# Optimization experiments

Measured on AMD Instinct MI355X. Metric: run time of the kernel, lower is better.

Reference implementation:

```python
import jax, jax.numpy as jnp
import numpy as np

ALPHA = 0.2   # LeakyReLU slope
NEG = -9e15   # masked-attention fill, as in standard dense GAT


def _gat_multihead(h, edge_attr, adj, n2n, Wg, Weg, a_s, a_d, a_e, concat):
    # h: [N, I], edge_attr: [E, I], adj: [N, N], n2n: [N*N, I]
    # Wg, Weg: [H, I, O]; a_s, a_d, a_e: [H, O]
    H, I, O = Wg.shape
    N = h.shape[0]
    Wh = jnp.einsum('ni,hio->hno', h, Wg)                    # [H, N, O]
    es = jnp.einsum('hno,ho->hn', Wh, a_s)                   # [H, N] source logits
    ed = jnp.einsum('hno,ho->hn', Wh, a_d)                   # [H, N] dest logits
    ve = jnp.einsum('hio,ho->hi', Weg, a_e)                  # [H, I] fold edge proj into vector
    ee = (n2n @ ve.T).T.reshape(H, N, N)                     # [H, N, N] edge logits (row=src)
    e = jax.nn.leaky_relu(es[:, :, None] + ed[:, None, :] + ee, ALPHA)
    e = jnp.where(adj[None] > 0, e, NEG)
    attn = jax.nn.softmax(e, axis=-1)
    hout = jnp.einsum('hnm,hmo->nho', attn, Wh).reshape(N, H * O)
    eout = jnp.einsum('ei,hio->eho', edge_attr, Weg).reshape(-1, H * O)
    if concat:
        hout, eout = jax.nn.elu(hout), jax.nn.elu(eout)
    return hout, eout


def _edge_pool(x, edge_index, edge_attr, Wp, bp):
    # Deterministic static-shape variant of EdgePooling: merge node pairs (2k, 2k+1)
    # with a learned sigmoid score over the concatenated endpoint features.
    N, F = x.shape
    x2 = x.reshape(N // 2, 2, F)
    score = jax.nn.sigmoid(jnp.concatenate([x2[:, 0], x2[:, 1]], axis=1) @ Wp + bp)  # [N/2,1]
    new_x = (x2[:, 0] + x2[:, 1]) * score
    return new_x, edge_index // 2, edge_attr


def _global_attn(x, W, b):
    # GlobalAttention with gate_nn = Linear -> Sigmoid, softmax over the single graph
    gate = jax.nn.sigmoid(x @ W + b)          # [N, 1]
    alpha = jax.nn.softmax(gate, axis=0)
    return (alpha * x).sum(axis=0, keepdims=True)  # [1, F]


def _adj_n2n(N, edge_index, edge_attr):
    # Faithful vectorized version of _get_adj_node2node (scatter replaces python loop)
    src, dst = edge_index[0], edge_index[1]
    adj = jnp.zeros((N, N), edge_attr.dtype).at[src, dst].add(1.0)
    n2n = jnp.zeros((N * N, edge_attr.shape[1]), edge_attr.dtype).at[src * N + dst].set(edge_attr)
    return adj, n2n


def setup_inputs() -> dict:
    key = jax.random.key(0)
    ks = jax.random.split(key, 24)
    N, E, HID, NH = 512, 4096, 64, 16
    O = 2 * HID                                  # per-head GAT output = 128
    CAT = NH * O                                 # 2048
    s = 0.1
    features = jax.random.normal(ks[0], (N, HID), jnp.float32)
    edge_index = jax.random.randint(ks[1], (2, E), 0, N, jnp.int64)
    edge_attr = jax.random.normal(ks[2], (E, HID), jnp.float32)
    adjacency, n2n = _adj_n2n(N, edge_index, edge_attr)
    inp = dict(features=features, edge_index=edge_index, edge_attr=edge_attr,
               adjacency=adjacency, n2n=n2n)
    # SingleNodeAttentionLayer params
    inp['W_sn'] = jax.random.normal(ks[3], (HID, HID), jnp.float32) * s
    inp['a_sn'] = jax.random.normal(ks[4], (HID,), jnp.float32) * s
    # 16-head GAT layer (stacked over heads)
    inp['Wg'] = jax.random.normal(ks[5], (NH, HID, O), jnp.float32) * s
    inp['Weg'] = jax.random.normal(ks[6], (NH, HID, O), jnp.float32) * s
    inp['a_src'] = jax.random.normal(ks[7], (NH, O), jnp.float32) * s
    inp['a_dst'] = jax.random.normal(ks[8], (NH, O), jnp.float32) * s
    inp['a_edge'] = jax.random.normal(ks[9], (NH, O), jnp.float32) * s
    # edge_pool1 (in = NH*O = 2048)
    inp['Wp1'] = jax.random.normal(ks[10], (2 * CAT, 1), jnp.float32) * s
    inp['bp1'] = jnp.zeros((1,), jnp.float32)
    # out_att single head: 2048 -> 128
    inp['Wo'] = jax.random.normal(ks[11], (CAT, O), jnp.float32) * s
    inp['Weo'] = jax.random.normal(ks[12], (CAT, O), jnp.float32) * s
    inp['ao_src'] = jax.random.normal(ks[13], (O,), jnp.float32) * s
    inp['ao_dst'] = jax.random.normal(ks[14], (O,), jnp.float32) * s
    inp['ao_edge'] = jax.random.normal(ks[15], (O,), jnp.float32) * s
    # edge_pool2 (in = O = 128)
    inp['Wp2'] = jax.random.normal(ks[16], (2 * O, 1), jnp.float32) * s
    inp['bp2'] = jnp.zeros((1,), jnp.float32)
    # global-attention gates
    inp['g1W'] = jax.random.normal(ks[17], (HID, 1), jnp.float32) * s
    inp['g1b'] = jnp.zeros((1,), jnp.float32)
    inp['g2W'] = jax.random.normal(ks[18], (CAT, 1), jnp.float32) * s
    inp['g2b'] = jnp.zeros((1,), jnp.float32)
    inp['g3W'] = jax.random.normal(ks[19], (O, 1), jnp.float32) * s
    inp['g3b'] = jnp.zeros((1,), jnp.float32)
    return inp


def reference(features, edge_index, edge_attr, adjacency, n2n,
              W_sn, a_sn, Wg, Weg, a_src, a_dst, a_edge, Wp1, bp1,
              Wo, Weo, ao_src, ao_dst, ao_edge, Wp2, bp2,
              g1W, g1b, g2W, g2b, g3W, g3b):
    # SingleNodeAttentionLayer: per-node gated projection
    Wh0 = features @ W_sn
    coef = jax.nn.sigmoid(jax.nn.leaky_relu(Wh0 @ a_sn, ALPHA))
    h = jax.nn.elu(coef[:, None] * Wh0)                       # [N, HID]
    hs = [_global_attn(h, g1W, g1b)]
    # 16-head GAT (dropout inactive: training=False)
    h, ea = _gat_multihead(h, edge_attr, adjacency, n2n, Wg, Weg, a_src, a_dst, a_edge, True)
    h, ei, ea = _edge_pool(h, edge_index, ea, Wp1, bp1)
    hs.append(_global_attn(h, g2W, g2b))
    # rebuild dense adjacency + node2node features (scatter)
    adj2, n2n2 = _adj_n2n(h.shape[0], ei, ea)
    h, ea = _gat_multihead(h, ea, adj2, n2n2, Wo[None], Weo[None],
                           ao_src[None], ao_dst[None], ao_edge[None], False)
    h, ei, ea = _edge_pool(h, ei, ea, Wp2, bp2)
    hs.append(_global_attn(h, g3W, g3b))
    return jnp.concatenate(hs, axis=1)                        # [1, 64+2048+128]
```

## Files before the change

### kernel.cpp

```cpp
#include <hip/hip_runtime.h>
#include <hip/hip_bf16.h>

__device__ __forceinline__ float sigm(float x) { return 1.f / (1.f + expf(-x)); }
__device__ __forceinline__ float lrelu(float x) { return x > 0.f ? x : 0.2f * x; }
__device__ __forceinline__ float eluf(float x) { return x > 0.f ? x : expf(x) - 1.f; }

#define NEGF (-9e15f)
#define MAXD 40

__device__ __forceinline__ float wave_sum(float v) {
    #pragma unroll
    for (int off = 32; off >= 1; off >>= 1) v += __shfl_xor(v, off);
    return v;
}
__device__ __forceinline__ float wave_max(float v) {
    #pragma unroll
    for (int off = 32; off >= 1; off >>= 1) v = fmaxf(v, __shfl_xor(v, off));
    return v;
}
__device__ __forceinline__ float half_sum(float v) {
    #pragma unroll
    for (int off = 16; off >= 1; off >>= 1) v += __shfl_xor(v, off);
    return v;
}
__device__ __forceinline__ float half_max(float v) {
    #pragma unroll
    for (int off = 16; off >= 1; off >>= 1) v = fmaxf(v, __shfl_xor(v, off));
    return v;
}

__global__ void k_setup(const float* __restrict__ Wg, const float* __restrict__ Weg,
                        const float* __restrict__ asrc, const float* __restrict__ adst,
                        const float* __restrict__ aedge, const float* __restrict__ Weo,
                        const float* __restrict__ aoe,
                        const float* __restrict__ feat, const float* __restrict__ Wsn,
                        const float* __restrict__ asn, const float* __restrict__ g1W,
                        const float* __restrict__ g1b,
                        float* __restrict__ vs1, float* __restrict__ vd1, float* __restrict__ ve1,
                        float* __restrict__ ve2, int* __restrict__ winner,
                        float* __restrict__ h, float* __restrict__ gate1) {
    int b = blockIdx.x, t = threadIdx.x, w = t >> 6, l = t & 63;
    __shared__ float fr[4][64];
    if (b < 16) {
        int hd = b;
        float s0 = asrc[hd * 128 + l],  s1 = asrc[hd * 128 + 64 + l];
        float d0 = adst[hd * 128 + l],  d1 = adst[hd * 128 + 64 + l];
        float e0 = aedge[hd * 128 + l], e1 = aedge[hd * 128 + 64 + l];
        for (int i = w; i < 64; i += 4) {
            const float* Wr = Wg  + ((size_t)hd * 64 + i) * 128;
            const float* Er = Weg + ((size_t)hd * 64 + i) * 128;
            float w1 = Wr[l], w2 = Wr[64 + l];
            float q1 = Er[l], q2 = Er[64 + l];
            float pS = wave_sum(w1 * s0 + w2 * s1);
            float pD = wave_sum(w1 * d0 + w2 * d1);
            float pE = wave_sum(q1 * e0 + q2 * e1);
            if (l == 0) { vs1[hd * 64 + i] = pS; vd1[hd * 64 + i] = pD; ve1[hd * 64 + i] = pE; }
        }
    } else if (b < 32) {
        int base = (b - 16) * 128;
        float a0 = aoe[l], a1 = aoe[64 + l];
        for (int k = 0; k < 32; k++) {
            int c = base + w * 32 + k;
            const float* Wr = Weo + (size_t)c * 128;
            float p = wave_sum(Wr[l] * a0 + Wr[64 + l] * a1);
            if (l == 0) ve2[c] = p;
        }
    } else if (b < 48) {
        int base = (b - 32) * 4096;
        #pragma unroll
        for (int k = 0; k < 16; k++) winner[base + k * 256 + t] = -1;
    } else {
        int n = (b - 48) * 4 + w;
        fr[w][l] = feat[n * 64 + l];
        __syncthreads();
        float acc = 0.f;
        #pragma unroll 8
        for (int i = 0; i < 64; i++) acc += fr[w][i] * Wsn[i * 64 + l];
        float p = wave_sum(acc * asn[l]);
        float coef = sigm(lrelu(p));
        float hv = eluf(coef * acc);
        h[n * 64 + l] = hv;
        float g = wave_sum(hv * g1W[l]);
        if (l == 0) gate1[n] = sigm(g + g1b[0]);
    }
}

__global__ void k_mid(const float* __restrict__ h, const float* __restrict__ gate,
                      const float* __restrict__ vs1, const float* __restrict__ vd1,
                      const int* __restrict__ ei,
                      float* __restrict__ part1, float* __restrict__ es1, float* __restrict__ ed1,
                      int* __restrict__ winner) {
    int b = blockIdx.x, t = threadIdx.x;
    if (b < 8) {
        int nb = b, w = t >> 6, l = t & 63;
        __shared__ float mx[8], sm[8], al[512], pt[8][64];
        float g = gate[t];
        float m = wave_max(g);
        if (l == 0) mx[w] = m;
        __syncthreads();
        m = mx[0];
        #pragma unroll
        for (int i = 1; i < 8; i++) m = fmaxf(m, mx[i]);
        float p = expf(g - m);
        float Z = wave_sum(p);
        if (l == 0) sm[w] = Z;
        __syncthreads();
        Z = 0.f;
        #pragma unroll
        for (int i = 0; i < 8; i++) Z += sm[i];
        al[t] = p / Z;
        __syncthreads();
        int r0 = nb * 64 + w * 8;
        float acc = 0.f;
        #pragma unroll
        for (int r = 0; r < 8; r++) acc += al[r0 + r] * h[(r0 + r) * 64 + l];
        pt[w][l] = acc;
        __syncthreads();
        if (t < 64) {
            float o = 0.f;
            #pragma unroll
            for (int q = 0; q < 8; q++) o += pt[q][t];
            part1[nb * 64 + t] = o;
        }
    } else if (b < 24) {
        __shared__ float vsT[64][17], vdT[64][17];
        for (int idx = t; idx < 1024; idx += 512) {
            int i = idx & 63, hd = idx >> 6;
            vsT[i][hd] = vs1[hd * 64 + i];
            vdT[i][hd] = vd1[hd * 64 + i];
        }
        __syncthreads();
        int idx = (b - 8) * 512 + t;
        int n = idx >> 4, hd = idx & 15;
        const float* hr = h + n * 64;
        float aS = 0.f, aD = 0.f;
        #pragma unroll 8
        for (int i = 0; i < 64; i++) {
            float hv = hr[i];
            aS += hv * vsT[i][hd];
            aD += hv * vdT[i][hd];
        }
        es1[hd * 512 + n] = aS;
        ed1[hd * 512 + n] = aD;
    } else {
        int e = (b - 24) * 512 + t;
        int s = ei[e] >> 1, d = ei[4096 + e] >> 1;
        atomicMax(&winner[s * 256 + d], e);
    }
}

__global__ void k_attn_ze(const float* __restrict__ adj, const float* __restrict__ n2n,
                          const float* __restrict__ h, const float* __restrict__ ve1,
                          const float* __restrict__ es1, const float* __restrict__ ed1,
                          const float* __restrict__ eattr, const float* __restrict__ Weg,
                          const float* __restrict__ ve2,
                          float* __restrict__ z, float* __restrict__ d2) {
    int b = blockIdx.x, t = threadIdx.x, w = t >> 6, l = t & 63;
    if (b >= 512) {
        int e0 = (b - 512) * 8;
        int hd = t >> 5, q = t & 31;
        __shared__ float ea[8][64];
        __shared__ float sd2[8][8];
        ea[t >> 6][t & 63] = eattr[(size_t)(e0 + (t >> 6)) * 64 + (t & 63)];
        __syncthreads();
        float4 acc[8];
        #pragma unroll
        for (int r = 0; r < 8; r++) acc[r] = make_float4(0.f, 0.f, 0.f, 0.f);
        const float4* W4 = (const float4*)Weg + (size_t)hd * 2048 + q;
        #pragma unroll 4
        for (int i = 0; i < 64; i++) {
            float4 wv = W4[i * 32];
            #pragma unroll
            for (int r = 0; r < 8; r++) {
                float a = ea[r][i];
                acc[r].x += a * wv.x; acc[r].y += a * wv.y;
                acc[r].z += a * wv.z; acc[r].w += a * wv.w;
            }
        }
        float4 v2 = ((const float4*)ve2)[hd * 32 + q];
        #pragma unroll
        for (int r = 0; r < 8; r++) {
            float p = eluf(acc[r].x) * v2.x + eluf(acc[r].y) * v2.y
                    + eluf(acc[r].z) * v2.z + eluf(acc[r].w) * v2.w;
            p = wave_sum(p);
            if (l == 0) sd2[r][w] = p;
        }
        __syncthreads();
        if (t < 8) {
            float s8 = 0.f;
            #pragma unroll
            for (int k = 0; k < 8; k++) s8 += sd2[t][k];
            d2[e0 + t] = s8;
        }
        return;
    }
    int s = b;
    __shared__ float vlT[64][17];
    __shared__ float hrow[MAXD][65], nrow[MAXD][65];
    __shared__ float eh[16][48], ah[16][48];
    __shared__ float esr[16];
    __shared__ int dlist[MAXD];
    __shared__ int wbase[8];
    __shared__ int nnz_s;
    __shared__ float part[8][64];

    for (int idx = t; idx < 1024; idx += 512) vlT[idx & 63][idx >> 6] = ve1[(idx >> 6) * 64 + (idx & 63)];
    if (t < 16) esr[t] = es1[t * 512 + s];
    float a = adj[s * 512 + t];
    unsigned long long mask = __ballot(a > 0.f);
    if (l == 0) wbase[w] = __popcll(mask);
    __syncthreads();
    if (t == 0) {
        int run = 0;
        #pragma unroll
        for (int i = 0; i < 8; i++) { int c = wbase[i]; wbase[i] = run; run += c; }
        nnz_s = run;
    }
    __syncthreads();
    if (a > 0.f) {
        int slot = wbase[w] + __popcll(mask & ((1ULL << l) - 1ULL));
        if (slot < MAXD) dlist[slot] = t;
    }
    __syncthreads();
    int nnz = min(nnz_s, MAXD);

    if (nnz == 0) {
        int i = t & 63, q = t >> 6;
        float acc = 0.f;
        for (int d = q * 64; d < q * 64 + 64; d++) acc += h[d * 64 + i];
        part[q][i] = acc;
        __syncthreads();
        if (t < 64) {
            float sum = 0.f;
            #pragma unroll
            for (int q2 = 0; q2 < 8; q2++) sum += part[q2][t];
            float v = sum * (1.f / 512.f);
            for (int hd = 0; hd < 16; hd++) z[(size_t)s * 1024 + hd * 64 + t] = v;
        }
        return;
    }

    for (int base = 0; base < nnz; base += 8) {
        int j = base + (t >> 6);
        if (j < nnz) {
            int d = dlist[j];
            hrow[j][l] = h[d * 64 + l];
            nrow[j][l] = n2n[((size_t)s * 512 + d) * 64 + l];
        }
    }
    __syncthreads();
    for (int jb = 0; jb < nnz; jb += 32) {
        int j = jb + (t >> 4), hd = t & 15;
        if (j < nnz) {
            float ee = 0.f;
            #pragma unroll 8
            for (int i = 0; i < 64; i++) ee += nrow[j][i] * vlT[i][hd];
            eh[hd][j] = lrelu(esr[hd] + ed1[hd * 512 + dlist[j]] + ee);
        }
    }
    __syncthreads();
    {
        int hd = t >> 5, lane32 = t & 31;
        float v0 = (lane32 < nnz) ? eh[hd][lane32] : -1e30f;
        float v1 = (lane32 + 32 < nnz) ? eh[hd][lane32 + 32] : -1e30f;
        float m = half_max(fmaxf(v0, v1));
        float p0 = (lane32 < nnz) ? expf(v0 - m) : 0.f;
        float p1 = (lane32 + 32 < nnz) ? expf(v1 - m) : 0.f;
        float Z = half_sum(p0 + p1);
        float inv = 1.f / Z;
        if (lane32 < nnz) ah[hd][lane32] = p0 * inv;
        if (lane32 + 32 < nnz) ah[hd][lane32 + 32] = p1 * inv;
    }
    __syncthreads();
    int hd = t >> 5, i0 = t & 31;
    float a0 = 0.f, a1 = 0.f;
    for (int j = 0; j < nnz; j++) {
        float aj = ah[hd][j];
        a0 += aj * hrow[j][i0];
        a1 += aj * hrow[j][i0 + 32];
    }
    z[(size_t)s * 1024 + hd * 64 + i0]      = a0;
    z[(size_t)s * 1024 + hd * 64 + i0 + 32] = a1;
}

__global__ void k_houtg(const float* __restrict__ z, const float* __restrict__ Wg,
                        float* __restrict__ hout) {
    int sb = blockIdx.x, hd = blockIdx.y, c = threadIdx.x;
    __shared__ float zt[8][64];
    int s0 = sb * 8;
    for (int idx = c; idx < 512; idx += 128) {
        int r = idx >> 6, i = idx & 63;
        zt[r][i] = z[(size_t)(s0 + r) * 1024 + hd * 64 + i];
    }
    __syncthreads();
    float acc[8] = {0, 0, 0, 0, 0, 0, 0, 0};
    const float* W = Wg + (size_t)hd * 8192 + c;
    #pragma unroll 8
    for (int i = 0; i < 64; i++) {
        float wv = W[(size_t)i * 128];
        #pragma unroll
        for (int r = 0; r < 8; r++) acc[r] += zt[r][i] * wv;
    }
    #pragma unroll
    for (int r = 0; r < 8; r++)
        hout[(size_t)(s0 + r) * 2048 + hd * 128 + c] = eluf(acc[r]);
}

__global__ void k_pool1g2(const float* __restrict__ x, const float* __restrict__ Wp,
                          const float* __restrict__ bp, const float* __restrict__ g2W,
                          const float* __restrict__ g2b,
                          float* __restrict__ xo, float* __restrict__ gate2) {
    int k = blockIdx.x, t = threadIdx.x, w = t >> 6, l = t & 63;
    __shared__ float sd[4], sg[4];
    float p = 0.f;
    for (int f = t; f < 2048; f += 256)
        p += x[(size_t)(2 * k) * 2048 + f] * Wp[f] + x[(size_t)(2 * k + 1) * 2048 + f] * Wp[2048 + f];
    p = wave_sum(p);
    if (l == 0) sd[w] = p;
    __syncthreads();
    float sc = sigm(sd[0] + sd[1] + sd[2] + sd[3] + bp[0]);
    float pg = 0.f;
    for (int f = t; f < 2048; f += 256) {
        float v = x[(size_t)(2 * k) * 2048 + f] + x[(size_t)(2 * k + 1) * 2048 + f];
        xo[(size_t)k * 2048 + f] = v * sc;
        pg += v * g2W[f];
    }
    pg = wave_sum(pg);
    if (l == 0) sg[w] = pg;
    __syncthreads();
    if (t == 0) gate2[k] = sigm(sc * (sg[0] + sg[1] + sg[2] + sg[3]) + g2b[0]);
}

__global__ void k_big2(const float* __restrict__ x, const float* __restrict__ Wo,
                       const float* __restrict__ aos, const float* __restrict__ aod,
                       const float* __restrict__ gate2,
                       float* __restrict__ Wh2, float* __restrict__ es2, float* __restrict__ ed2,
                       float* __restrict__ part2) {
    int b = blockIdx.x, t = threadIdx.x;
    if (b < 128) {
        int n0 = b * 2;
        int ks = t >> 7, c = t & 127;
        __shared__ float xr[2][2048];
        __shared__ float part[8][2][128];
        __shared__ float rs[4], rd[4];
        for (int idx = t; idx < 4096; idx += 1024) xr[idx >> 11][idx & 2047] = x[(size_t)n0 * 2048 + idx];
        __syncthreads();
        float a0 = 0.f, a1 = 0.f;
        const float* W  = Wo + (size_t)(ks * 256) * 128 + c;
        const float* x0 = xr[0] + ks * 256;
        const float* x1 = xr[1] + ks * 256;
        #pragma unroll 8
        for (int i = 0; i < 256; i++) { float w = W[(size_t)i * 128]; a0 += x0[i] * w; a1 += x1[i] * w; }
        part[ks][0][c] = a0;
        part[ks][1][c] = a1;
        __syncthreads();
        if (t < 256) {
            int r = t >> 7, cc = t & 127;
            float a = 0.f;
            #pragma unroll
            for (int k = 0; k < 8; k++) a += part[k][r][cc];
            Wh2[(n0 + r) * 128 + cc] = a;
            float ps = wave_sum(a * aos[cc]);
            float pd = wave_sum(a * aod[cc]);
            if ((t & 63) == 0) { rs[t >> 6] = ps; rd[t >> 6] = pd; }
        }
        __syncthreads();
        if (t == 0) { es2[n0] = rs[0] + rs[1]; ed2[n0] = rd[0] + rd[1]; }
        if (t == 1) { es2[n0 + 1] = rs[2] + rs[3]; ed2[n0 + 1] = rd[2] + rd[3]; }
    } else {
        int wb = b - 128;
        int grp = t >> 8, tt = t & 255;
        int tile = wb * 4 + grp;
        int cb = tile >> 3, nb = tile & 7;
        __shared__ float mx[4][4], sm[4][4], al[4][256];
        int w4 = tt >> 6, l = tt & 63;
        float g = gate2[tt];
        float m = wave_max(g);
        if (l == 0) mx[grp][w4] = m;
        __syncthreads();
        m = fmaxf(fmaxf(mx[grp][0], mx[grp][1]), fmaxf(mx[grp][2], mx[grp][3]));
        float p = expf(g - m);
        float Z = wave_sum(p);
        if (l == 0) sm[grp][w4] = Z;
        __syncthreads();
        Z = sm[grp][0] + sm[grp][1] + sm[grp][2] + sm[grp][3];
        al[grp][tt] = p / Z;
        __syncthreads();
        int c = cb * 256 + tt;
        int n0 = nb * 32;
        float acc = 0.f;
        #pragma unroll 8
        for (int n = n0; n < n0 + 32; n++) acc += al[grp][n] * x[(size_t)n * 2048 + c];
        part2[nb * 2048 + c] = acc;
    }
}

__global__ void k_fin(const int* __restrict__ winner, const float* __restrict__ d2,
                      const float* __restrict__ es2, const float* __restrict__ ed2,
                      const float* __restrict__ Wh2, const float* __restrict__ part1,
                      const float* __restrict__ part2,
                      float* __restrict__ hout2, float* __restrict__ out) {
    int b = blockIdx.x, t = threadIdx.x;
    if (b < 256) {
        int s = b, w = t >> 6, l = t & 63;
        __shared__ float mx[4], sm[4], at[256], part[2][128];
        int win = winner[s * 256 + t];
        float e;
        if (win >= 0) e = lrelu(es2[s] + ed2[t] + d2[win]);
        else e = NEGF;
        float m = wave_max(e);
        if (l == 0) mx[w] = m;
        __syncthreads();
        m = fmaxf(fmaxf(mx[0], mx[1]), fmaxf(mx[2], mx[3]));
        float p = expf(e - m);
        float Z = wave_sum(p);
        if (l == 0) sm[w] = Z;
        __syncthreads();
        Z = sm[0] + sm[1] + sm[2] + sm[3];
        at[t] = p / Z;
        __syncthreads();
        int c = t & 127, hf = t >> 7;
        float acc = 0.f;
        for (int d = hf * 128; d < hf * 128 + 128; d++)
            acc += at[d] * Wh2[d * 128 + c];
        part[hf][c] = acc;
        __syncthreads();
        if (t < 128) hout2[s * 128 + t] = part[0][t] + part[1][t];
    } else if (b == 256) {
        if (t < 64) {
            float o = 0.f;
            #pragma unroll
            for (int nb = 0; nb < 8; nb++) o += part1[nb * 64 + t];
            out[t] = o;
        }
    } else {
        int c = (b - 257) * 256 + t;
        float o = 0.f;
        #pragma unroll
        for (int nb = 0; nb < 8; nb++) o += part2[nb * 2048 + c];
        out[64 + c] = o;
    }
}

__global__ void k_tail(const float* __restrict__ hout2, const float* __restrict__ Wp,
                       const float* __restrict__ bp, const float* __restrict__ g3W,
                       const float* __restrict__ g3b, float* __restrict__ out) {
    int t = threadIdx.x, w = t >> 6, l = t & 63;
    __shared__ float x2s[128][129];
    __shared__ float gt[128];
    __shared__ float mx[2], sm[2], al[128], part[4][128];
    float bpv = bp[0], g3bv = g3b[0];
    for (int rr = 0; rr < 16; rr++) {
        int k = w * 16 + rr;
        float a0  = hout2[(size_t)(2 * k) * 128 + l];
        float a0b = hout2[(size_t)(2 * k) * 128 + 64 + l];
        float a1  = hout2[(size_t)(2 * k + 1) * 128 + l];
        float a1b = hout2[(size_t)(2 * k + 1) * 128 + 64 + l];
        float p = a0 * Wp[l] + a0b * Wp[64 + l] + a1 * Wp[128 + l] + a1b * Wp[192 + l];
        p = wave_sum(p);
        float sc = sigm(p + bpv);
        float v  = (a0 + a1) * sc;
        float vb = (a0b + a1b) * sc;
        x2s[k][l] = v;
        x2s[k][64 + l] = vb;
        float g = wave_sum(v * g3W[l] + vb * g3W[64 + l]);
        if (l == 0) gt[k] = sigm(g + g3bv);
    }
    __syncthreads();
    if (t < 128) {
        float g = gt[t];
        float m = wave_max(g);
        if (l == 0) mx[w] = m;
    }
    __syncthreads();
    if (t < 128) {
        float g = gt[t];
        float m = fmaxf(mx[0], mx[1]);
        float p = expf(g - m);
        float Z = wave_sum(p);
        if (l == 0) sm[w] = Z;
        al[t] = p;
    }
    __syncthreads();
    float invZ = 1.f / (sm[0] + sm[1]);
    int q = t >> 7, c = t & 127;
    float acc = 0.f;
    for (int n = q * 32; n < q * 32 + 32; n++) acc += al[n] * x2s[n][c];
    part[q][c] = acc * invZ;
    __syncthreads();
    if (t < 128) out[2112 + t] = part[0][t] + part[1][t] + part[2][t] + part[3][t];
}

extern "C" void kernel_launch(void* const* d_in, const int* in_sizes, int n_in,
                              void* d_out, int out_size, void* d_ws, size_t ws_size,
                              hipStream_t stream) {
    const float* feat  = (const float*)d_in[0];
    const int*   eidx  = (const int*)d_in[1];
    const float* eattr = (const float*)d_in[2];
    const float* adj   = (const float*)d_in[3];
    const float* n2n   = (const float*)d_in[4];
    const float* Wsn   = (const float*)d_in[5];
    const float* asn   = (const float*)d_in[6];
    const float* Wg    = (const float*)d_in[7];
    const float* Weg   = (const float*)d_in[8];
    const float* asrc  = (const float*)d_in[9];
    const float* adst  = (const float*)d_in[10];
    const float* aedge = (const float*)d_in[11];
    const float* Wp1   = (const float*)d_in[12];
    const float* bp1   = (const float*)d_in[13];
    const float* Wo    = (const float*)d_in[14];
    const float* Weo   = (const float*)d_in[15];
    const float* aos   = (const float*)d_in[16];
    const float* aod   = (const float*)d_in[17];
    const float* aoe   = (const float*)d_in[18];
    const float* Wp2   = (const float*)d_in[19];
    const float* bp2   = (const float*)d_in[20];
    const float* g1W   = (const float*)d_in[21];
    const float* g1b   = (const float*)d_in[22];
    const float* g2W   = (const float*)d_in[23];
    const float* g2b   = (const float*)d_in[24];
    const float* g3W   = (const float*)d_in[25];
    const float* g3b   = (const float*)d_in[26];
    float* out = (float*)d_out;

    char* ws = (char*)d_ws;
    float* h      = (float*)(ws + 0x0000000);
    float* z      = (float*)(ws + 0x0020000);
    float* ve1    = (float*)(ws + 0x0430000);
    float* ve2    = (float*)(ws + 0x0431000);
    float* gate1  = (float*)(ws + 0x0433000);
    float* gate2  = (float*)(ws + 0x0434000);
    float* vs1    = (float*)(ws + 0x0436000);
    float* vd1    = (float*)(ws + 0x0438000);
    float* es1    = (float*)(ws + 0x0440000);
    float* ed1    = (float*)(ws + 0x0448000);
    float* hout1  = (float*)(ws + 0x1440000);
    float* d2     = (float*)(ws + 0x1840000);
    float* x1p    = (float*)(ws + 0x1850000);
    int*   winner = (int*)  (ws + 0x1A50000);
    float* Wh2    = (float*)(ws + 0x1A90000);
    float* es2    = (float*)(ws + 0x1AB0000);
    float* ed2    = (float*)(ws + 0x1AB1000);
    float* hout2  = (float*)(ws + 0x1AB2000);
    float* part2  = (float*)(ws + 0x1AE2000);
    float* part1  = (float*)(ws + 0x1AF2000);

    k_setup  <<<176, 256, 0, stream>>>(Wg, Weg, asrc, adst, aedge, Weo, aoe,
                                       feat, Wsn, asn, g1W, g1b,
                                       vs1, vd1, ve1, ve2, winner, h, gate1);
    k_mid    <<<32, 512, 0, stream>>>(h, gate1, vs1, vd1, eidx, part1, es1, ed1, winner);
    k_attn_ze<<<1024, 512, 0, stream>>>(adj, n2n, h, ve1, es1, ed1, eattr, Weg, ve2, z, d2);
    k_houtg  <<<dim3(64, 16), 128, 0, stream>>>(z, Wg, hout1);
    k_pool1g2<<<256, 256, 0, stream>>>(hout1, Wp1, bp1, g2W, g2b, x1p, gate2);
    k_big2   <<<144, 1024, 0, stream>>>(x1p, Wo, aos, aod, gate2, Wh2, es2, ed2, part2);
    k_fin    <<<265, 256, 0, stream>>>(winner, d2, es2, ed2, Wh2, part1, part2, hout2, out);
    k_tail   <<<1, 512, 0, stream>>>(hout2, Wp2, bp2, g3W, g3b, out);
}
```

Measured before the change: 130.9 us.

## Restage edge projection per head, fuse pool1 into big2, rebalance later kernels

The edge-projection branch of k_attn_ze now runs one block per (head, 256-edge chunk). Each block keeps that head's Weg slice in shared memory and writes per-head partial d2 values. k_houtg gains an extra row of blocks that reduces those partials across heads. k_pool1g2 is folded into k_big2p, so pooled rows come straight from shared memory instead of a separate launch. The global-attention partial sums move into k_fin and the final out reduction into extra k_tail blocks, which removes one launch at the cost of an extra workspace buffer and more shared memory per block.

```diff
diff --git a/kernel.cpp b/kernel.cpp
--- a/kernel.cpp
+++ b/kernel.cpp
@@ -154,55 +154,46 @@
                           const float* __restrict__ es1, const float* __restrict__ ed1,
                           const float* __restrict__ eattr, const float* __restrict__ Weg,
                           const float* __restrict__ ve2,
-                          float* __restrict__ z, float* __restrict__ d2) {
+                          float* __restrict__ z, float* __restrict__ d2p) {
     int b = blockIdx.x, t = threadIdx.x, w = t >> 6, l = t & 63;
+    __shared__ __align__(16) char smem[34816];
     if (b >= 512) {
-        int e0 = (b - 512) * 8;
-        int hd = t >> 5, q = t & 31;
-        __shared__ float ea[8][64];
-        __shared__ float sd2[8][8];
-        ea[t >> 6][t & 63] = eattr[(size_t)(e0 + (t >> 6)) * 64 + (t & 63)];
-        __syncthreads();
-        float4 acc[8];
-        #pragma unroll
-        for (int r = 0; r < 8; r++) acc[r] = make_float4(0.f, 0.f, 0.f, 0.f);
-        const float4* W4 = (const float4*)Weg + (size_t)hd * 2048 + q;
-        #pragma unroll 4
-        for (int i = 0; i < 64; i++) {
-            float4 wv = W4[i * 32];
-            #pragma unroll
-            for (int r = 0; r < 8; r++) {
-                float a = ea[r][i];
-                acc[r].x += a * wv.x; acc[r].y += a * wv.y;
-                acc[r].z += a * wv.z; acc[r].w += a * wv.w;
+        float (*Wl)[128] = reinterpret_cast<float(*)[128]>(smem);
+        float (*ea8)[64] = reinterpret_cast<float(*)[64]>(smem + 32768);
+        int bb = b - 512;
+        int hd = bb & 15, e0 = (bb >> 4) * 256;
+        for (int idx = t; idx < 8192; idx += 512)
+            Wl[idx >> 7][idx & 127] = Weg[(size_t)hd * 8192 + idx];
+        float v2a = ve2[hd * 128 + l];
+        float v2b = ve2[hd * 128 + 64 + l];
+        for (int ebase = 0; ebase < 256; ebase += 8) {
+            __syncthreads();
+            ea8[t >> 6][t & 63] = eattr[(size_t)(e0 + ebase + (t >> 6)) * 64 + (t & 63)];
+            __syncthreads();
+            float a0 = 0.f, a1 = 0.f;
+            #pragma unroll 8
+            for (int i = 0; i < 64; i++) {
+                float r = ea8[w][i];
+                a0 += r * Wl[i][l];
+                a1 += r * Wl[i][64 + l];
             }
-        }
-        float4 v2 = ((const float4*)ve2)[hd * 32 + q];
-        #pragma unroll
-        for (int r = 0; r < 8; r++) {
-            float p = eluf(acc[r].x) * v2.x + eluf(acc[r].y) * v2.y
-                    + eluf(acc[r].z) * v2.z + eluf(acc[r].w) * v2.w;
+            float p = eluf(a0) * v2a + eluf(a1) * v2b;
             p = wave_sum(p);
-            if (l == 0) sd2[r][w] = p;
-        }
-        __syncthreads();
-        if (t < 8) {
-            float s8 = 0.f;
-            #pragma unroll
-            for (int k = 0; k < 8; k++) s8 += sd2[t][k];
-            d2[e0 + t] = s8;
+            if (l == 0) d2p[hd * 4096 + e0 + ebase + w] = p;
         }
         return;
     }
     int s = b;
-    __shared__ float vlT[64][17];
-    __shared__ float hrow[MAXD][65], nrow[MAXD][65];
-    __shared__ float eh[16][48], ah[16][48];
-    __shared__ float esr[16];
-    __shared__ int dlist[MAXD];
-    __shared__ int wbase[8];
-    __shared__ int nnz_s;
-    __shared__ float part[8][64];
+    float (*vlT)[17]  = reinterpret_cast<float(*)[17]>(smem);
+    float (*hrow)[65] = reinterpret_cast<float(*)[65]>(smem + 4352);
+    float (*nrow)[65] = reinterpret_cast<float(*)[65]>(smem + 14752);
+    float (*eh)[48]   = reinterpret_cast<float(*)[48]>(smem + 25152);
+    float (*ah)[48]   = reinterpret_cast<float(*)[48]>(smem + 28224);
+    float *esr        = reinterpret_cast<float*>(smem + 31296);
+    int   *dlist      = reinterpret_cast<int*>(smem + 31360);
+    int   *wbase      = reinterpret_cast<int*>(smem + 31520);
+    int   *nnz_sp     = reinterpret_cast<int*>(smem + 31552);
+    float (*part)[64] = reinterpret_cast<float(*)[64]>(smem + 31568);
 
     for (int idx = t; idx < 1024; idx += 512) vlT[idx & 63][idx >> 6] = ve1[(idx >> 6) * 64 + (idx & 63)];
     if (t < 16) esr[t] = es1[t * 512 + s];
@@ -214,7 +205,7 @@
         int run = 0;
         #pragma unroll
         for (int i = 0; i < 8; i++) { int c = wbase[i]; wbase[i] = run; run += c; }
-        nnz_s = run;
+        nnz_sp[0] = run;
     }
     __syncthreads();
     if (a > 0.f) {
@@ -222,7 +213,7 @@
         if (slot < MAXD) dlist[slot] = t;
     }
     __syncthreads();
-    int nnz = min(nnz_s, MAXD);
+    int nnz = min(nnz_sp[0], MAXD);
 
     if (nnz == 0) {
         int i = t & 63, q = t >> 6;
@@ -284,8 +275,19 @@
 }
 
 __global__ void k_houtg(const float* __restrict__ z, const float* __restrict__ Wg,
-                        float* __restrict__ hout) {
+                        const float* __restrict__ d2p,
+                        float* __restrict__ hout, float* __restrict__ d2) {
     int sb = blockIdx.x, hd = blockIdx.y, c = threadIdx.x;
+    if (hd == 16) {
+        if (c < 64) {
+            int e = sb * 64 + c;
+            float s = 0.f;
+            #pragma unroll
+            for (int k = 0; k < 16; k++) s += d2p[k * 4096 + e];
+            d2[e] = s;
+        }
+        return;
+    }
     __shared__ float zt[8][64];
     int s0 = sb * 8;
     for (int idx = c; idx < 512; idx += 128) {
@@ -306,100 +308,79 @@
         hout[(size_t)(s0 + r) * 2048 + hd * 128 + c] = eluf(acc[r]);
 }
 
-__global__ void k_pool1g2(const float* __restrict__ x, const float* __restrict__ Wp,
-                          const float* __restrict__ bp, const float* __restrict__ g2W,
-                          const float* __restrict__ g2b,
-                          float* __restrict__ xo, float* __restrict__ gate2) {
-    int k = blockIdx.x, t = threadIdx.x, w = t >> 6, l = t & 63;
-    __shared__ float sd[4], sg[4];
+__global__ void k_big2p(const float* __restrict__ hout1, const float* __restrict__ Wp1,
+                        const float* __restrict__ bp1, const float* __restrict__ g2W,
+                        const float* __restrict__ g2b, const float* __restrict__ Wo,
+                        const float* __restrict__ aos, const float* __restrict__ aod,
+                        float* __restrict__ x1p, float* __restrict__ gate2,
+                        float* __restrict__ Wh2, float* __restrict__ es2, float* __restrict__ ed2) {
+    int b = blockIdx.x, t = threadIdx.x;
+    __shared__ float hs[4][2048];
+    __shared__ float xr[2][2048];
+    __shared__ float part[8][2][128];
+    __shared__ float red[16], rs[4], rd[4];
+    int n0 = 2 * b;
+    for (int idx = t; idx < 8192; idx += 1024)
+        hs[idx >> 11][idx & 2047] = hout1[(size_t)(4 * b) * 2048 + idx];
+    __syncthreads();
+    int g = t >> 9, tt = t & 511;
     float p = 0.f;
-    for (int f = t; f < 2048; f += 256)
-        p += x[(size_t)(2 * k) * 2048 + f] * Wp[f] + x[(size_t)(2 * k + 1) * 2048 + f] * Wp[2048 + f];
+    for (int f = tt; f < 2048; f += 512)
+        p += hs[2 * g][f] * Wp1[f] + hs[2 * g + 1][f] * Wp1[2048 + f];
     p = wave_sum(p);
-    if (l == 0) sd[w] = p;
-    __syncthreads();
-    float sc = sigm(sd[0] + sd[1] + sd[2] + sd[3] + bp[0]);
+    if ((t & 63) == 0) red[t >> 6] = p;
+    __syncthreads();
+    float s8 = 0.f;
+    #pragma unroll
+    for (int k2 = 0; k2 < 8; k2++) s8 += red[g * 8 + k2];
+    float sc = sigm(s8 + bp1[0]);
+    __syncthreads();
     float pg = 0.f;
-    for (int f = t; f < 2048; f += 256) {
-        float v = x[(size_t)(2 * k) * 2048 + f] + x[(size_t)(2 * k + 1) * 2048 + f];
-        xo[(size_t)k * 2048 + f] = v * sc;
+    for (int f = tt; f < 2048; f += 512) {
+        float v = (hs[2 * g][f] + hs[2 * g + 1][f]) * sc;
+        xr[g][f] = v;
+        x1p[(size_t)(n0 + g) * 2048 + f] = v;
         pg += v * g2W[f];
     }
     pg = wave_sum(pg);
-    if (l == 0) sg[w] = pg;
-    __syncthreads();
-    if (t == 0) gate2[k] = sigm(sc * (sg[0] + sg[1] + sg[2] + sg[3]) + g2b[0]);
-}
-
-__global__ void k_big2(const float* __restrict__ x, const float* __restrict__ Wo,
-                       const float* __restrict__ aos, const float* __restrict__ aod,
-                       const float* __restrict__ gate2,
-                       float* __restrict__ Wh2, float* __restrict__ es2, float* __restrict__ ed2,
-                       float* __restrict__ part2) {
-    int b = blockIdx.x, t = threadIdx.x;
-    if (b < 128) {
-        int n0 = b * 2;
-        int ks = t >> 7, c = t & 127;
-        __shared__ float xr[2][2048];
-        __shared__ float part[8][2][128];
-        __shared__ float rs[4], rd[4];
-        for (int idx = t; idx < 4096; idx += 1024) xr[idx >> 11][idx & 2047] = x[(size_t)n0 * 2048 + idx];
-        __syncthreads();
-        float a0 = 0.f, a1 = 0.f;
-        const float* W  = Wo + (size_t)(ks * 256) * 128 + c;
-        const float* x0 = xr[0] + ks * 256;
-        const float* x1 = xr[1] + ks * 256;
-        #pragma unroll 8
-        for (int i = 0; i < 256; i++) { float w = W[(size_t)i * 128]; a0 += x0[i] * w; a1 += x1[i] * w; }
-        part[ks][0][c] = a0;
-        part[ks][1][c] = a1;
-        __syncthreads();
-        if (t < 256) {
-            int r = t >> 7, cc = t & 127;
-            float a = 0.f;
-            #pragma unroll
-            for (int k = 0; k < 8; k++) a += part[k][r][cc];
-            Wh2[(n0 + r) * 128 + cc] = a;
-            float ps = wave_sum(a * aos[cc]);
-            float pd = wave_sum(a * aod[cc]);
-            if ((t & 63) == 0) { rs[t >> 6] = ps; rd[t >> 6] = pd; }
-        }
-        __syncthreads();
-        if (t == 0) { es2[n0] = rs[0] + rs[1]; ed2[n0] = rd[0] + rd[1]; }
-        if (t == 1) { es2[n0 + 1] = rs[2] + rs[3]; ed2[n0 + 1] = rd[2] + rd[3]; }
-    } else {
-        int wb = b - 128;
-        int grp = t >> 8, tt = t & 255;
-        int tile = wb * 4 + grp;
-        int cb = tile >> 3, nb = tile & 7;
-        __shared__ float mx[4][4], sm[4][4], al[4][256];
-        int w4 = tt >> 6, l = tt & 63;
-        float g = gate2[tt];
-        float m = wave_max(g);
-        if (l == 0) mx[grp][w4] = m;
-        __syncthreads();
-        m = fmaxf(fmaxf(mx[grp][0], mx[grp][1]), fmaxf(mx[grp][2], mx[grp][3]));
-        float p = expf(g - m);
-        float Z = wave_sum(p);
-        if (l == 0) sm[grp][w4] = Z;
-        __syncthreads();
-        Z = sm[grp][0] + sm[grp][1] + sm[grp][2] + sm[grp][3];
-        al[grp][tt] = p / Z;
-        __syncthreads();
-        int c = cb * 256 + tt;
-        int n0 = nb * 32;
-        float acc = 0.f;
-        #pragma unroll 8
-        for (int n = n0; n < n0 + 32; n++) acc += al[grp][n] * x[(size_t)n * 2048 + c];
-        part2[nb * 2048 + c] = acc;
-    }
+    if ((t & 63) == 0) red[t >> 6] = pg;
+    __syncthreads();
+    if (t == 0 || t == 512) {
+        float sg8 = 0.f;
+        #pragma unroll
+        for (int k2 = 0; k2 < 8; k2++) sg8 += red[g * 8 + k2];
+        gate2[n0 + g] = sigm(sg8 + g2b[0]);
+    }
+    int ks = t >> 7, c = t & 127;
+    float a0 = 0.f, a1 = 0.f;
+    const float* W  = Wo + (size_t)(ks * 256) * 128 + c;
+    const float* x0 = xr[0] + ks * 256;
+    const float* x1 = xr[1] + ks * 256;
+    #pragma unroll 8
+    for (int i = 0; i < 256; i++) { float w = W[(size_t)i * 128]; a0 += x0[i] * w; a1 += x1[i] * w; }
+    part[ks][0][c] = a0;
+    part[ks][1][c] = a1;
+    __syncthreads();
+    if (t < 256) {
+        int r = t >> 7, cc = t & 127;
+        float a = 0.f;
+        #pragma unroll
+        for (int k2 = 0; k2 < 8; k2++) a += part[k2][r][cc];
+        Wh2[(n0 + r) * 128 + cc] = a;
+        float ps = wave_sum(a * aos[cc]);
+        float pd = wave_sum(a * aod[cc]);
+        if ((t & 63) == 0) { rs[t >> 6] = ps; rd[t >> 6] = pd; }
+    }
+    __syncthreads();
+    if (t == 0) { es2[n0] = rs[0] + rs[1]; ed2[n0] = rd[0] + rd[1]; }
+    if (t == 1) { es2[n0 + 1] = rs[2] + rs[3]; ed2[n0 + 1] = rd[2] + rd[3]; }
 }
 
 __global__ void k_fin(const int* __restrict__ winner, const float* __restrict__ d2,
                       const float* __restrict__ es2, const float* __restrict__ ed2,
-                      const float* __restrict__ Wh2, const float* __restrict__ part1,
-                      const float* __restrict__ part2,
-                      float* __restrict__ hout2, float* __restrict__ out) {
+                      const float* __restrict__ Wh2, const float* __restrict__ gate2,
+                      const float* __restrict__ x1p,
+                      float* __restrict__ part2, float* __restrict__ hout2) {
     int b = blockIdx.x, t = threadIdx.x;
     if (b < 256) {
         int s = b, w = t >> 6, l = t & 63;
@@ -426,26 +407,55 @@
         part[hf][c] = acc;
         __syncthreads();
         if (t < 128) hout2[s * 128 + t] = part[0][t] + part[1][t];
-    } else if (b == 256) {
-        if (t < 64) {
+    } else {
+        int tile = b - 256;
+        int cb = tile >> 3, nb = tile & 7;
+        __shared__ float mx2[4], sm2[4], al[256];
+        int w = t >> 6, l = t & 63;
+        float g = gate2[t];
+        float m = wave_max(g);
+        if (l == 0) mx2[w] = m;
+        __syncthreads();
+        m = fmaxf(fmaxf(mx2[0], mx2[1]), fmaxf(mx2[2], mx2[3]));
+        float p = expf(g - m);
+        float Z = wave_sum(p);
+        if (l == 0) sm2[w] = Z;
+        __syncthreads();
+        Z = sm2[0] + sm2[1] + sm2[2] + sm2[3];
+        al[t] = p / Z;
+        __syncthreads();
+        int c = cb * 256 + t;
+        int n0 = nb * 32;
+        float acc = 0.f;
+        #pragma unroll 8
+        for (int n = n0; n < n0 + 32; n++) acc += al[n] * x1p[(size_t)n * 2048 + c];
+        part2[nb * 2048 + c] = acc;
+    }
+}
+
+__global__ void k_tail(const float* __restrict__ hout2, const float* __restrict__ Wp,
+                       const float* __restrict__ bp, const float* __restrict__ g3W,
+                       const float* __restrict__ g3b, const float* __restrict__ part1,
+                       const float* __restrict__ part2, float* __restrict__ out) {
+    int t = threadIdx.x, w = t >> 6, l = t & 63;
+    if (blockIdx.x > 0) {
+        int rb = blockIdx.x - 1;
+        if (rb == 0) {
+            if (t < 64) {
+                float o = 0.f;
+                #pragma unroll
+                for (int nb = 0; nb < 8; nb++) o += part1[nb * 64 + t];
+                out[t] = o;
+            }
+        } else if (t < 256) {
+            int c = (rb - 1) * 256 + t;
             float o = 0.f;
             #pragma unroll
-            for (int nb = 0; nb < 8; nb++) o += part1[nb * 64 + t];
-            out[t] = o;
-        }
-    } else {
-        int c = (b - 257) * 256 + t;
-        float o = 0.f;
-        #pragma unroll
-        for (int nb = 0; nb < 8; nb++) o += part2[nb * 2048 + c];
-        out[64 + c] = o;
-    }
-}
-
-__global__ void k_tail(const float* __restrict__ hout2, const float* __restrict__ Wp,
-                       const float* __restrict__ bp, const float* __restrict__ g3W,
-                       const float* __restrict__ g3b, float* __restrict__ out) {
-    int t = threadIdx.x, w = t >> 6, l = t & 63;
+            for (int nb = 0; nb < 8; nb++) o += part2[nb * 2048 + c];
+            out[64 + c] = o;
+        }
+        return;
+    }
     __shared__ float x2s[128][129];
     __shared__ float gt[128];
     __shared__ float mx[2], sm[2], al[128], part[4][128];
@@ -534,6 +544,7 @@
     float* vd1    = (float*)(ws + 0x0438000);
     float* es1    = (float*)(ws + 0x0440000);
     float* ed1    = (float*)(ws + 0x0448000);
+    float* d2p    = (float*)(ws + 0x0500000);
     float* hout1  = (float*)(ws + 0x1440000);
     float* d2     = (float*)(ws + 0x1840000);
     float* x1p    = (float*)(ws + 0x1850000);
@@ -549,10 +560,10 @@
                                        feat, Wsn, asn, g1W, g1b,
                                        vs1, vd1, ve1, ve2, winner, h, gate1);
     k_mid    <<<32, 512, 0, stream>>>(h, gate1, vs1, vd1, eidx, part1, es1, ed1, winner);
-    k_attn_ze<<<1024, 512, 0, stream>>>(adj, n2n, h, ve1, es1, ed1, eattr, Weg, ve2, z, d2);
-    k_houtg  <<<dim3(64, 16), 128, 0, stream>>>(z, Wg, hout1);
-    k_pool1g2<<<256, 256, 0, stream>>>(hout1, Wp1, bp1, g2W, g2b, x1p, gate2);
-    k_big2   <<<144, 1024, 0, stream>>>(x1p, Wo, aos, aod, gate2, Wh2, es2, ed2, part2);
-    k_fin    <<<265, 256, 0, stream>>>(winner, d2, es2, ed2, Wh2, part1, part2, hout2, out);
-    k_tail   <<<1, 512, 0, stream>>>(hout2, Wp2, bp2, g3W, g3b, out);
-}
+    k_attn_ze<<<768, 512, 0, stream>>>(adj, n2n, h, ve1, es1, ed1, eattr, Weg, ve2, z, d2p);
+    k_houtg  <<<dim3(64, 17), 128, 0, stream>>>(z, Wg, d2p, hout1, d2);
+    k_big2p  <<<128, 1024, 0, stream>>>(hout1, Wp1, bp1, g2W, g2b, Wo, aos, aod,
+                                        x1p, gate2, Wh2, es2, ed2);
+    k_fin    <<<320, 256, 0, stream>>>(winner, d2, es2, ed2, Wh2, gate2, x1p, part2, hout2);
+    k_tail   <<<10, 512, 0, stream>>>(hout2, Wp2, bp2, g3W, g3b, part1, part2, out);
+}
```

Measured after the change: 163.3 us. 24.7% more time.
